# Performance work log

Measured on AMD Instinct MI355X. Metric: run time of the kernel, lower is better.

Reference implementation:

```python
import jax, jax.numpy as jnp
import numpy as np

MARGIN = 0.4
SCALE = 80.0
NEG_FILL = -1e30  # used instead of -inf for masked logsumexp (keeps grads NaN-free)

N, D, NUM_CLASSES = 8192, 128, 512


def setup_inputs() -> dict:
    key = jax.random.key(0)
    k1, k2 = jax.random.split(key)
    embeds = jax.random.normal(k1, (N, D), dtype=jnp.float32)
    labels = jax.random.randint(k2, (N,), 0, NUM_CLASSES, dtype=jnp.int64)
    return {"embeds": embeds, "labels": labels}


def _masked_lse(terms, mask):
    # stable logsumexp over axis=1 restricted to mask
    t = jnp.where(mask, terms, NEG_FILL)
    m = jnp.max(t, axis=1, keepdims=True)
    return jnp.squeeze(m, 1) + jnp.log(jnp.sum(jnp.exp(t - m), axis=1))


def reference(embeds, labels):
    # L2-normalize embeddings (F.normalize, p=2, dim=1, eps=1e-12)
    norm = jnp.maximum(jnp.linalg.norm(embeds, axis=1, keepdims=True), 1e-12)
    e = embeds / norm
    sim = e @ e.T  # [N, N]

    same = labels[:, None] == labels[None, :]
    eye = jnp.eye(labels.shape[0], dtype=bool)
    pos_mask = same & ~eye          # positives for each anchor (row)
    neg_mask = ~same                # negatives for each anchor

    # alphas are computed under no_grad in the original
    ap_alpha = jax.lax.stop_gradient(jax.nn.relu(1.0 + MARGIN - sim))
    an_alpha = jax.lax.stop_gradient(jax.nn.relu(sim + MARGIN))

    ap_term = -SCALE * ap_alpha * (sim - 1.0 + MARGIN)
    an_term = SCALE * an_alpha * (sim - MARGIN)

    np_cnt = jnp.sum(pos_mask, axis=1)  # positives per anchor
    nn_cnt = jnp.sum(neg_mask, axis=1)  # negatives per anchor
    valid = (np_cnt > 0) & (nn_cnt > 0)

    # All-triplets logsumexp factorizes: LSE over (p,n) pairs of ap_term[p]
    # equals LSE over p + log(num_neg); symmetric for an_term.
    lse_p = _masked_lse(ap_term, pos_mask)
    lse_n = _masked_lse(an_term, neg_mask)
    log_np = jnp.where(valid, jnp.log(np_cnt.astype(sim.dtype)), 0.0)
    log_nn = jnp.where(valid, jnp.log(nn_cnt.astype(sim.dtype)), 0.0)

    loss_i = jax.nn.softplus(lse_p + log_nn + lse_n + log_np)
    loss = jnp.sum(jnp.where(valid, loss_i, 0.0)) / jnp.maximum(
        jnp.sum(valid).astype(sim.dtype), 1.0)
    return loss
```

## Files before the change

### kernel.cpp

```cpp
#include <hip/hip_runtime.h>
#include <hip/hip_bf16.h>

#define NN_ 8192
#define DD_ 128
#define NSPLIT 8
#define JSPLIT (NN_ / NSPLIT)

typedef short bf16x8 __attribute__((ext_vector_type(8)));
typedef float f32x4 __attribute__((ext_vector_type(4)));

union U4 { uint4 u; bf16x8 h; };

#if __has_builtin(__builtin_amdgcn_exp2f)
#define EXP2(x) __builtin_amdgcn_exp2f(x)
#else
#define EXP2(x) __expf((x) * 0.69314718056f)
#endif

#define C1 115.415603f
#define C2 96.9491065f
#define LN2 0.69314718056f

__device__ __forceinline__ unsigned short f2bf(float f) {
    unsigned int u = __float_as_uint(f);
    unsigned int r = (u + 0x7FFFu + ((u >> 16) & 1u)) >> 16;
    return (unsigned short)r;
}


__global__ __launch_bounds__(256) void k_norm(const float* __restrict__ x,
                                              unsigned short* __restrict__ ebf) {
    int t = threadIdx.x;
    int r16 = t >> 4;
    int g = t & 15;
    int row = blockIdx.x * 16 + r16;
    const float4* xr = (const float4*)(x + (size_t)row * DD_);
    float4 v0 = xr[g * 2];
    float4 v1 = xr[g * 2 + 1];
    float ss = v0.x * v0.x + v0.y * v0.y + v0.z * v0.z + v0.w * v0.w +
               v1.x * v1.x + v1.y * v1.y + v1.z * v1.z + v1.w * v1.w;
#pragma unroll
    for (int m = 16; m < 256; m <<= 1) {
    }
#pragma unroll
    for (int m = 1; m < 16; m <<= 1) ss += __shfl_xor(ss, m);
    float inv = 1.0f / fmaxf(sqrtf(ss), 1e-12f);
    float vs[8] = {v0.x, v0.y, v0.z, v0.w, v1.x, v1.y, v1.z, v1.w};
    unsigned int p[4];
#pragma unroll
    for (int k = 0; k < 4; k++) {
        unsigned short lo = f2bf(vs[2 * k] * inv);
        unsigned short hi = f2bf(vs[2 * k + 1] * inv);
        p[k] = (unsigned int)lo | ((unsigned int)hi << 16);
    }
    uint4 out = {p[0], p[1], p[2], p[3]};
    ((uint4*)ebf)[blockIdx.x * 256 + g * 16 + r16] = out;
}

__global__ __launch_bounds__(512, 4) void k_main(const unsigned short* __restrict__ ebf,
                                                 const int* __restrict__ labels,
                                                 float* __restrict__ states) {
    const int lane = threadIdx.x & 63;
    const int wave = threadIdx.x >> 6;
    const int quad = lane >> 4;
    const int lcol = lane & 15;
    const int rowbase = blockIdx.y * 128 + wave * 16;
    const int jsplit = blockIdx.x;
    const int j0 = jsplit * JSPLIT, j1 = j0 + JSPLIT;

    const uint4* fb = (const uint4*)ebf;

    U4 afr[4];
#pragma unroll
    for (int kc = 0; kc < 4; kc++) afr[kc].u = fb[(rowbase >> 4) * 256 + kc * 64 + lane];

    int il[4];
#pragma unroll
    for (int r = 0; r < 4; r++) il[r] = labels[rowbase + quad * 4 + r];

    float S_an[4] = {0.f, 0.f, 0.f, 0.f};
    float m_p[4] = {-1e30f, -1e30f, -1e30f, -1e30f};
    float s_p[4] = {0.f, 0.f, 0.f, 0.f};
    float cnt[4] = {0.f, 0.f, 0.f, 0.f};

    U4 b0[4], b1[4];
#pragma unroll
    for (int kc = 0; kc < 4; kc++) b0[kc].u = fb[(j0 >> 4) * 256 + kc * 64 + lane];
    int jl0 = labels[j0 + lcol];
#pragma unroll
    for (int kc = 0; kc < 4; kc++) b1[kc].u = fb[((j0 + 16) >> 4) * 256 + kc * 64 + lane];
    int jl1 = labels[j0 + 16 + lcol];

    const int NIT = JSPLIT / 32;
    for (int it = 0; it < NIT; ++it) {
        const int jt = j0 + it * 32;
        const int jp = (it + 1 < NIT) ? jt + 32 : j0;

        {
            f32x4 acc = {0.f, 0.f, 0.f, 0.f};
#pragma unroll
            for (int kc = 0; kc < 4; kc++)
                acc = __builtin_amdgcn_mfma_f32_16x16x32_bf16(afr[kc].h, b0[kc].h, acc, 0, 0, 0);
            int j = jt + lcol;
#pragma unroll
            for (int r = 0; r < 4; r++) {
                float s = acc[r];
                int i = rowbase + quad * 4 + r;
                bool same = (jl0 == il[r]);
                float u = s + 0.4f;
                float a = fmaxf(u, 0.0f);
                float t2 = fmaf(a * C1, u - 0.8f, -C2);
                float e = EXP2(t2);
                S_an[r] += same ? 0.0f : e;
                cnt[r] += same ? 1.0f : 0.0f;
                if (same && j != i) {
                    float al = fmaxf(1.4f - s, 0.0f) * (-C1);
                    float tp = al * (s - 0.6f);
                    float mn = fmaxf(m_p[r], tp);
                    s_p[r] = s_p[r] * EXP2(m_p[r] - mn) + EXP2(tp - mn);
                    m_p[r] = mn;
                }
            }
        }
#pragma unroll
        for (int kc = 0; kc < 4; kc++) b0[kc].u = fb[(jp >> 4) * 256 + kc * 64 + lane];
        int jl0n = labels[jp + lcol];

        {
            f32x4 acc = {0.f, 0.f, 0.f, 0.f};
#pragma unroll
            for (int kc = 0; kc < 4; kc++)
                acc = __builtin_amdgcn_mfma_f32_16x16x32_bf16(afr[kc].h, b1[kc].h, acc, 0, 0, 0);
            int j = jt + 16 + lcol;
#pragma unroll
            for (int r = 0; r < 4; r++) {
                float s = acc[r];
                int i = rowbase + quad * 4 + r;
                bool same = (jl1 == il[r]);
                float u = s + 0.4f;
                float a = fmaxf(u, 0.0f);
                float t2 = fmaf(a * C1, u - 0.8f, -C2);
                float e = EXP2(t2);
                S_an[r] += same ? 0.0f : e;
                cnt[r] += same ? 1.0f : 0.0f;
                if (same && j != i) {
                    float al = fmaxf(1.4f - s, 0.0f) * (-C1);
                    float tp = al * (s - 0.6f);
                    float mn = fmaxf(m_p[r], tp);
                    s_p[r] = s_p[r] * EXP2(m_p[r] - mn) + EXP2(tp - mn);
                    m_p[r] = mn;
                }
            }
        }
#pragma unroll
        for (int kc = 0; kc < 4; kc++) b1[kc].u = fb[((jp + 16) >> 4) * 256 + kc * 64 + lane];
        int jl1n = labels[jp + 16 + lcol];

        jl0 = jl0n;
        jl1 = jl1n;
    }

#pragma unroll
    for (int r = 0; r < 4; r++) {
#pragma unroll
        for (int m = 1; m < 16; m <<= 1) {
            S_an[r] += __shfl_xor(S_an[r], m);
            cnt[r] += __shfl_xor(cnt[r], m);
            float m2 = __shfl_xor(m_p[r], m);
            float s2 = __shfl_xor(s_p[r], m);
            float mn = fmaxf(m_p[r], m2);
            s_p[r] = s_p[r] * EXP2(m_p[r] - mn) + s2 * EXP2(m2 - mn);
            m_p[r] = mn;
        }
    }
    if (lcol == 0) {
#pragma unroll
        for (int r = 0; r < 4; r++) {
            int i = rowbase + quad * 4 + r;
            float4 st = {m_p[r], s_p[r], S_an[r], cnt[r]};
            ((float4*)states)[(size_t)i * NSPLIT + jsplit] = st;
        }
    }
}

__global__ __launch_bounds__(256) void k_fin(const float* __restrict__ states,
                                             float* __restrict__ partials) {
    int i = blockIdx.x * 256 + threadIdx.x;
    float m_p = -1e30f, s_p = 0.f, S_an = 0.f, cnt = 0.f;
#pragma unroll
    for (int k = 0; k < NSPLIT; k++) {
        float4 st = ((const float4*)states)[(size_t)i * NSPLIT + k];
        S_an += st.z;
        cnt += st.w;
        float mn = fmaxf(m_p, st.x);
        s_p = s_p * EXP2(m_p - mn) + st.y * EXP2(st.x - mn);
        m_p = mn;
    }
    int np = (int)cnt - 1;
    int nn = NN_ - (int)cnt;
    float loss = 0.0f, v = 0.0f;
    if (np > 0 && nn > 0 && s_p > 0.f && S_an > 0.f) {
        float lse_p = LN2 * m_p + __logf(s_p);
        float lse_n = 67.2f + __logf(S_an);
        float z = lse_p + lse_n + __logf((float)np) + __logf((float)nn);
        loss = fmaxf(z, 0.0f) + log1pf(__expf(-fabsf(z)));
        v = 1.0f;
    }
#pragma unroll
    for (int m = 1; m < 64; m <<= 1) {
        loss += __shfl_xor(loss, m);
        v += __shfl_xor(v, m);
    }
    if ((threadIdx.x & 63) == 0) {
        int w = (blockIdx.x << 2) | (threadIdx.x >> 6);
        partials[w * 2] = loss;
        partials[w * 2 + 1] = v;
    }
}

__global__ void k_div(const float* __restrict__ partials, float* __restrict__ out) {
    int t = threadIdx.x;
    float loss = partials[t * 2] + partials[(t + 64) * 2];
    float v = partials[t * 2 + 1] + partials[(t + 64) * 2 + 1];
#pragma unroll
    for (int m = 1; m < 64; m <<= 1) {
        loss += __shfl_xor(loss, m);
        v += __shfl_xor(v, m);
    }
    if (t == 0) out[0] = loss / fmaxf(v, 1.0f);
}

extern "C" void kernel_launch(void* const* d_in, const int* in_sizes, int n_in,
                              void* d_out, int out_size, void* d_ws, size_t ws_size,
                              hipStream_t stream) {
    const float* embeds = (const float*)d_in[0];
    const int* labels = (const int*)d_in[1];
    float* out = (float*)d_out;

    char* ws = (char*)d_ws;
    unsigned short* ebf = (unsigned short*)ws;
    float* states = (float*)(ws + 2097152);
    float* partials = (float*)(ws + 2097152 + 1048576);

    k_norm<<<NN_ / 16, 256, 0, stream>>>(embeds, ebf);
    k_main<<<dim3(NSPLIT, NN_ / 128), 512, 0, stream>>>(ebf, labels, states);
    k_fin<<<NN_ / 256, 256, 0, stream>>>(states, partials);
    k_div<<<1, 64, 0, stream>>>(partials, out);
}
```

Baseline: 103.9 us.

## Sort rows by label so most tiles skip positive-pair and label checks

Adds a single-block counting-sort kernel that permutes rows by class label and records per-class start offsets. The normalize kernel writes embeddings in sorted order, and the main kernel computes each wave's label range. For column tiles outside that range it runs a reduced loop that only accumulates the negative exp term, skipping the label load, compare, count and positive logsumexp update. This trades an extra serial single-block launch and a scattered write for much less per-element ALU work in the hot loop.

After: 106.3 us. 2.3% more time.

```diff
diff --git a/kernel.cpp b/kernel.cpp
--- a/kernel.cpp
+++ b/kernel.cpp
@@ -3,6 +3,7 @@
 
 #define NN_ 8192
 #define DD_ 128
+#define NCLS 512
 #define NSPLIT 8
 #define JSPLIT (NN_ / NSPLIT)
 
@@ -28,7 +29,53 @@
 }
 
 
+__global__ __launch_bounds__(1024) void k_sort(const int* __restrict__ labels,
+                                               int* __restrict__ rowdest,
+                                               int* __restrict__ plab,
+                                               int* __restrict__ start) {
+    __shared__ int hist[NCLS];
+    __shared__ int base[NCLS];
+    __shared__ int wsum[8];
+    int t = threadIdx.x;
+    if (t < NCLS) hist[t] = 0;
+    __syncthreads();
+    int l[8];
+#pragma unroll
+    for (int k = 0; k < 8; k++) {
+        l[k] = labels[t * 8 + k];
+        atomicAdd(&hist[l[k]], 1);
+    }
+    __syncthreads();
+    int v = (t < NCLS) ? hist[t] : 0;
+    int x = v;
+#pragma unroll
+    for (int m = 1; m < 64; m <<= 1) {
+        int y = __shfl_up(x, m);
+        if ((t & 63) >= m) x += y;
+    }
+    if (t < NCLS && (t & 63) == 63) wsum[t >> 6] = x;
+    __syncthreads();
+    if (t < NCLS) {
+        int w = t >> 6, woff = 0;
+#pragma unroll
+        for (int k = 0; k < 8; k++)
+            if (k < w) woff += wsum[k];
+        int excl = woff + x - v;
+        start[t] = excl;
+        base[t] = excl;
+        if (t == 0) start[NCLS] = NN_;
+    }
+    __syncthreads();
+#pragma unroll
+    for (int k = 0; k < 8; k++) {
+        int p = atomicAdd(&base[l[k]], 1);
+        rowdest[t * 8 + k] = p;
+        plab[p] = l[k];
+    }
+}
+
 __global__ __launch_bounds__(256) void k_norm(const float* __restrict__ x,
+                                              const int* __restrict__ rowdest,
                                               unsigned short* __restrict__ ebf) {
     int t = threadIdx.x;
     int r16 = t >> 4;
@@ -40,9 +87,6 @@
     float ss = v0.x * v0.x + v0.y * v0.y + v0.z * v0.z + v0.w * v0.w +
                v1.x * v1.x + v1.y * v1.y + v1.z * v1.z + v1.w * v1.w;
 #pragma unroll
-    for (int m = 16; m < 256; m <<= 1) {
-    }
-#pragma unroll
     for (int m = 1; m < 16; m <<= 1) ss += __shfl_xor(ss, m);
     float inv = 1.0f / fmaxf(sqrtf(ss), 1e-12f);
     float vs[8] = {v0.x, v0.y, v0.z, v0.w, v1.x, v1.y, v1.z, v1.w};
@@ -54,11 +98,13 @@
         p[k] = (unsigned int)lo | ((unsigned int)hi << 16);
     }
     uint4 out = {p[0], p[1], p[2], p[3]};
-    ((uint4*)ebf)[blockIdx.x * 256 + g * 16 + r16] = out;
+    int d = rowdest[row];
+    ((uint4*)ebf)[(d >> 4) * 256 + g * 16 + (d & 15)] = out;
 }
 
 __global__ __launch_bounds__(512, 4) void k_main(const unsigned short* __restrict__ ebf,
-                                                 const int* __restrict__ labels,
+                                                 const int* __restrict__ plab,
+                                                 const int* __restrict__ start,
                                                  float* __restrict__ states) {
     const int lane = threadIdx.x & 63;
     const int wave = threadIdx.x >> 6;
@@ -66,7 +112,7 @@
     const int lcol = lane & 15;
     const int rowbase = blockIdx.y * 128 + wave * 16;
     const int jsplit = blockIdx.x;
-    const int j0 = jsplit * JSPLIT, j1 = j0 + JSPLIT;
+    const int j0 = jsplit * JSPLIT;
 
     const uint4* fb = (const uint4*)ebf;
 
@@ -76,7 +122,12 @@
 
     int il[4];
 #pragma unroll
-    for (int r = 0; r < 4; r++) il[r] = labels[rowbase + quad * 4 + r];
+    for (int r = 0; r < 4; r++) il[r] = plab[rowbase + quad * 4 + r];
+
+    int labmin = __builtin_amdgcn_readfirstlane(plab[rowbase]);
+    int labmax = __builtin_amdgcn_readfirstlane(plab[rowbase + 15]);
+    int lo = __builtin_amdgcn_readfirstlane(start[labmin]);
+    int hi = __builtin_amdgcn_readfirstlane(start[labmax + 1]);
 
     float S_an[4] = {0.f, 0.f, 0.f, 0.f};
     float m_p[4] = {-1e30f, -1e30f, -1e30f, -1e30f};
@@ -86,10 +137,8 @@
     U4 b0[4], b1[4];
 #pragma unroll
     for (int kc = 0; kc < 4; kc++) b0[kc].u = fb[(j0 >> 4) * 256 + kc * 64 + lane];
-    int jl0 = labels[j0 + lcol];
 #pragma unroll
     for (int kc = 0; kc < 4; kc++) b1[kc].u = fb[((j0 + 16) >> 4) * 256 + kc * 64 + lane];
-    int jl1 = labels[j0 + 16 + lcol];
 
     const int NIT = JSPLIT / 32;
     for (int it = 0; it < NIT; ++it) {
@@ -101,63 +150,75 @@
 #pragma unroll
             for (int kc = 0; kc < 4; kc++)
                 acc = __builtin_amdgcn_mfma_f32_16x16x32_bf16(afr[kc].h, b0[kc].h, acc, 0, 0, 0);
-            int j = jt + lcol;
-#pragma unroll
-            for (int r = 0; r < 4; r++) {
-                float s = acc[r];
-                int i = rowbase + quad * 4 + r;
-                bool same = (jl0 == il[r]);
-                float u = s + 0.4f;
-                float a = fmaxf(u, 0.0f);
-                float t2 = fmaf(a * C1, u - 0.8f, -C2);
-                float e = EXP2(t2);
-                S_an[r] += same ? 0.0f : e;
-                cnt[r] += same ? 1.0f : 0.0f;
-                if (same && j != i) {
-                    float al = fmaxf(1.4f - s, 0.0f) * (-C1);
-                    float tp = al * (s - 0.6f);
-                    float mn = fmaxf(m_p[r], tp);
-                    s_p[r] = s_p[r] * EXP2(m_p[r] - mn) + EXP2(tp - mn);
-                    m_p[r] = mn;
+            if (jt < hi && jt + 16 > lo) {
+                int jl = plab[jt + lcol];
+                int j = jt + lcol;
+#pragma unroll
+                for (int r = 0; r < 4; r++) {
+                    float s = acc[r];
+                    int i = rowbase + quad * 4 + r;
+                    bool same = (jl == il[r]);
+                    float a = fmaxf(s + 0.4f, 0.0f);
+                    float e = EXP2(fmaf(a * C1, s - 0.4f, -C2));
+                    S_an[r] += same ? 0.0f : e;
+                    cnt[r] += same ? 1.0f : 0.0f;
+                    if (same && j != i) {
+                        float al = fmaxf(1.4f - s, 0.0f) * (-C1);
+                        float tp = al * (s - 0.6f);
+                        float mn = fmaxf(m_p[r], tp);
+                        s_p[r] = s_p[r] * EXP2(m_p[r] - mn) + EXP2(tp - mn);
+                        m_p[r] = mn;
+                    }
+                }
+            } else {
+#pragma unroll
+                for (int r = 0; r < 4; r++) {
+                    float s = acc[r];
+                    float a = fmaxf(s + 0.4f, 0.0f);
+                    S_an[r] += EXP2(fmaf(a * C1, s - 0.4f, -C2));
                 }
             }
         }
 #pragma unroll
         for (int kc = 0; kc < 4; kc++) b0[kc].u = fb[(jp >> 4) * 256 + kc * 64 + lane];
-        int jl0n = labels[jp + lcol];
 
         {
             f32x4 acc = {0.f, 0.f, 0.f, 0.f};
 #pragma unroll
             for (int kc = 0; kc < 4; kc++)
                 acc = __builtin_amdgcn_mfma_f32_16x16x32_bf16(afr[kc].h, b1[kc].h, acc, 0, 0, 0);
-            int j = jt + 16 + lcol;
-#pragma unroll
-            for (int r = 0; r < 4; r++) {
-                float s = acc[r];
-                int i = rowbase + quad * 4 + r;
-                bool same = (jl1 == il[r]);
-                float u = s + 0.4f;
-                float a = fmaxf(u, 0.0f);
-                float t2 = fmaf(a * C1, u - 0.8f, -C2);
-                float e = EXP2(t2);
-                S_an[r] += same ? 0.0f : e;
-                cnt[r] += same ? 1.0f : 0.0f;
-                if (same && j != i) {
-                    float al = fmaxf(1.4f - s, 0.0f) * (-C1);
-                    float tp = al * (s - 0.6f);
-                    float mn = fmaxf(m_p[r], tp);
-                    s_p[r] = s_p[r] * EXP2(m_p[r] - mn) + EXP2(tp - mn);
-                    m_p[r] = mn;
+            const int jtt = jt + 16;
+            if (jtt < hi && jtt + 16 > lo) {
+                int jl = plab[jtt + lcol];
+                int j = jtt + lcol;
+#pragma unroll
+                for (int r = 0; r < 4; r++) {
+                    float s = acc[r];
+                    int i = rowbase + quad * 4 + r;
+                    bool same = (jl == il[r]);
+                    float a = fmaxf(s + 0.4f, 0.0f);
+                    float e = EXP2(fmaf(a * C1, s - 0.4f, -C2));
+                    S_an[r] += same ? 0.0f : e;
+                    cnt[r] += same ? 1.0f : 0.0f;
+                    if (same && j != i) {
+                        float al = fmaxf(1.4f - s, 0.0f) * (-C1);
+                        float tp = al * (s - 0.6f);
+                        float mn = fmaxf(m_p[r], tp);
+                        s_p[r] = s_p[r] * EXP2(m_p[r] - mn) + EXP2(tp - mn);
+                        m_p[r] = mn;
+                    }
+                }
+            } else {
+#pragma unroll
+                for (int r = 0; r < 4; r++) {
+                    float s = acc[r];
+                    float a = fmaxf(s + 0.4f, 0.0f);
+                    S_an[r] += EXP2(fmaf(a * C1, s - 0.4f, -C2));
                 }
             }
         }
 #pragma unroll
         for (int kc = 0; kc < 4; kc++) b1[kc].u = fb[((jp + 16) >> 4) * 256 + kc * 64 + lane];
-        int jl1n = labels[jp + 16 + lcol];
-
-        jl0 = jl0n;
-        jl1 = jl1n;
     }
 
 #pragma unroll
@@ -240,10 +301,14 @@
     char* ws = (char*)d_ws;
     unsigned short* ebf = (unsigned short*)ws;
     float* states = (float*)(ws + 2097152);
-    float* partials = (float*)(ws + 2097152 + 1048576);
-
-    k_norm<<<NN_ / 16, 256, 0, stream>>>(embeds, ebf);
-    k_main<<<dim3(NSPLIT, NN_ / 128), 512, 0, stream>>>(ebf, labels, states);
+    float* partials = (float*)(ws + 3145728);
+    int* rowdest = (int*)(ws + 3146752);
+    int* plab = (int*)(ws + 3179520);
+    int* start = (int*)(ws + 3212288);
+
+    k_sort<<<1, 1024, 0, stream>>>(labels, rowdest, plab, start);
+    k_norm<<<NN_ / 16, 256, 0, stream>>>(embeds, rowdest, ebf);
+    k_main<<<dim3(NSPLIT, NN_ / 128), 512, 0, stream>>>(ebf, plab, start, states);
     k_fin<<<NN_ / 256, 256, 0, stream>>>(states, partials);
     k_div<<<1, 64, 0, stream>>>(partials, out);
 }
```
